# Kernel tuning notes

Measured on AMD Instinct MI355X. Metric: run time of the kernel, lower is better.

The kernel has to match this reference:

```python
import jax, jax.numpy as jnp
import numpy as np

B = 49152  # batch, divisible by 3 so each class has exactly B//3 samples
D = 512    # embedding dim
MARGIN1 = 0.5
MARGIN2 = 1.0


def setup_inputs() -> dict:
    key = jax.random.key(0)
    k1, k2 = jax.random.split(key)
    true_label = jnp.arange(B, dtype=jnp.int32) % 3  # equal class counts
    embedding = jax.random.normal(k1, (B, D), dtype=jnp.float32)
    proto = jax.random.normal(k2, (D,), dtype=jnp.float32)
    return {"true_label": true_label, "embedding": embedding, "proto": proto}


def reference(true_label, embedding, proto):
    count = true_label.shape[0] // 3  # static: labels are balanced by construction
    # per-sample squared distance to the prototype: d_i = ||proto - e_i||^2, shape [B]
    d = jnp.sum((proto[None, :] - embedding) ** 2, axis=-1)
    # fixed-size index gathers (jit-compatible since each class has exactly `count` members)
    i0 = jnp.nonzero(true_label == 0, size=count)[0]
    i1 = jnp.nonzero(true_label == 1, size=count)[0]
    i2 = jnp.nonzero(true_label == 2, size=count)[0]
    d1, d2, d3 = d[i0], d[i1], d[i2]  # each [count]
    loss = (jax.nn.relu(d1 - d2 + MARGIN1)
            + jax.nn.relu(d2 - d3 + MARGIN1)
            + jax.nn.relu(d1 - d3 + MARGIN2))
    # loop summed per-cc scalar losses then divided by count == mean
    return jnp.mean(loss)
```

## Files before the change

kernel.cpp:

```cpp
#include <hip/hip_runtime.h>

#define MARGIN1 0.5f
#define MARGIN2 1.0f

__global__ __launch_bounds__(256) void soso_main_kernel(
    const int* __restrict__ lab,
    const float* __restrict__ emb,
    const float* __restrict__ proto,
    float* __restrict__ partial,
    int ngroups)
{
    const int lane = threadIdx.x & 63;
    const int wid  = threadIdx.x >> 6;
    const int wavesPerGrid = gridDim.x * 4;
    const int gwave = blockIdx.x * 4 + wid;

    const float4 p0 = *reinterpret_cast<const float4*>(proto + 4 * lane);
    const float4 p1 = *reinterpret_cast<const float4*>(proto + 256 + 4 * lane);

    float acc = 0.0f;

    for (int g = gwave; g < ngroups; g += wavesPerGrid) {
        const float* base = emb + (size_t)g * 3u * 512u;
        float dsum[3];
#pragma unroll
        for (int r = 0; r < 3; ++r) {
            const float* row = base + r * 512;
            const float4 e0 = *reinterpret_cast<const float4*>(row + 4 * lane);
            const float4 e1 = *reinterpret_cast<const float4*>(row + 256 + 4 * lane);
            float s = 0.0f, t;
            t = p0.x - e0.x; s = fmaf(t, t, s);
            t = p0.y - e0.y; s = fmaf(t, t, s);
            t = p0.z - e0.z; s = fmaf(t, t, s);
            t = p0.w - e0.w; s = fmaf(t, t, s);
            t = p1.x - e1.x; s = fmaf(t, t, s);
            t = p1.y - e1.y; s = fmaf(t, t, s);
            t = p1.z - e1.z; s = fmaf(t, t, s);
            t = p1.w - e1.w; s = fmaf(t, t, s);
#pragma unroll
            for (int off = 32; off > 0; off >>= 1)
                s += __shfl_xor(s, off, 64);
            dsum[r] = s;
        }
        const int l0 = lab[3 * g + 0];
        const int l1 = lab[3 * g + 1];
        const int l2 = lab[3 * g + 2];
        const float d1 = (l0 == 0) ? dsum[0] : (l1 == 0) ? dsum[1] : dsum[2];
        const float d2 = (l0 == 1) ? dsum[0] : (l1 == 1) ? dsum[1] : dsum[2];
        const float d3 = (l0 == 2) ? dsum[0] : (l1 == 2) ? dsum[1] : dsum[2];

        acc += fmaxf(d1 - d2 + MARGIN1, 0.0f)
             + fmaxf(d2 - d3 + MARGIN1, 0.0f)
             + fmaxf(d1 - d3 + MARGIN2, 0.0f);
    }

    __shared__ float smem[4];
    if (lane == 0) smem[wid] = acc;
    __syncthreads();
    if (threadIdx.x == 0)
        partial[blockIdx.x] = smem[0] + smem[1] + smem[2] + smem[3];
}

__global__ __launch_bounds__(256) void soso_reduce_kernel(
    const float* __restrict__ partial,
    float* __restrict__ out,
    int n,
    float inv_count)
{
    float s = 0.0f;
    for (int i = threadIdx.x; i < n; i += 256)
        s += partial[i];
#pragma unroll
    for (int off = 32; off > 0; off >>= 1)
        s += __shfl_xor(s, off, 64);
    __shared__ float smem[4];
    if ((threadIdx.x & 63) == 0) smem[threadIdx.x >> 6] = s;
    __syncthreads();
    if (threadIdx.x == 0)
        out[0] = (smem[0] + smem[1] + smem[2] + smem[3]) * inv_count;
}

extern "C" void kernel_launch(void* const* d_in, const int* in_sizes, int n_in,
                              void* d_out, int out_size, void* d_ws, size_t ws_size,
                              hipStream_t stream)
{
    const int*   lab   = (const int*)d_in[0];
    const float* emb   = (const float*)d_in[1];
    const float* proto = (const float*)d_in[2];
    float* out = (float*)d_out;

    const int B = in_sizes[0];
    const int ngroups = B / 3;

    float* partial = (float*)d_ws;
    const int blocks = 2048;

    soso_main_kernel<<<blocks, 256, 0, stream>>>(lab, emb, proto, partial, ngroups);
    soso_reduce_kernel<<<1, 256, 0, stream>>>(partial, out, blocks,
                                              1.0f / (float)ngroups);
}
```

Before: 23.35 us.

## Replace two-kernel reduction with atomicAdd and launch one wave per two groups

Drops the second reduction kernel. Each block now atomically adds its scaled partial sum into the output, which is zeroed with a memset beforehand. The grid-stride loop becomes a fixed mapping of two groups per wave with a grid sized to the problem (2048 blocks), and launch bounds now request 8 blocks per CU. This removes a kernel launch and the serial tail reduction, in exchange for a memset node and 2048 atomics contending on a single address, plus a float summation order that is no longer deterministic.

```diff
diff --git a/kernel.cpp b/kernel.cpp
--- a/kernel.cpp
+++ b/kernel.cpp
@@ -3,81 +3,68 @@
 #define MARGIN1 0.5f
 #define MARGIN2 1.0f
 
-__global__ __launch_bounds__(256) void soso_main_kernel(
+__global__ __launch_bounds__(256, 8) void soso_main_kernel(
     const int* __restrict__ lab,
     const float* __restrict__ emb,
     const float* __restrict__ proto,
-    float* __restrict__ partial,
-    int ngroups)
+    float* __restrict__ out,
+    int ngroups,
+    float inv_count)
 {
-    const int lane = threadIdx.x & 63;
-    const int wid  = threadIdx.x >> 6;
-    const int wavesPerGrid = gridDim.x * 4;
+    const int lane  = threadIdx.x & 63;
+    const int wid   = threadIdx.x >> 6;
     const int gwave = blockIdx.x * 4 + wid;
+    const int g0    = gwave * 2;
 
     const float4 p0 = *reinterpret_cast<const float4*>(proto + 4 * lane);
     const float4 p1 = *reinterpret_cast<const float4*>(proto + 256 + 4 * lane);
 
     float acc = 0.0f;
 
-    for (int g = gwave; g < ngroups; g += wavesPerGrid) {
-        const float* base = emb + (size_t)g * 3u * 512u;
-        float dsum[3];
 #pragma unroll
-        for (int r = 0; r < 3; ++r) {
-            const float* row = base + r * 512;
-            const float4 e0 = *reinterpret_cast<const float4*>(row + 4 * lane);
-            const float4 e1 = *reinterpret_cast<const float4*>(row + 256 + 4 * lane);
-            float s = 0.0f, t;
-            t = p0.x - e0.x; s = fmaf(t, t, s);
-            t = p0.y - e0.y; s = fmaf(t, t, s);
-            t = p0.z - e0.z; s = fmaf(t, t, s);
-            t = p0.w - e0.w; s = fmaf(t, t, s);
-            t = p1.x - e1.x; s = fmaf(t, t, s);
-            t = p1.y - e1.y; s = fmaf(t, t, s);
-            t = p1.z - e1.z; s = fmaf(t, t, s);
-            t = p1.w - e1.w; s = fmaf(t, t, s);
+    for (int gg = 0; gg < 2; ++gg) {
+        const int g = g0 + gg;
+        if (g < ngroups) {
+            const float* base = emb + (size_t)g * 1536u;
+            float ds[3];
 #pragma unroll
-            for (int off = 32; off > 0; off >>= 1)
-                s += __shfl_xor(s, off, 64);
-            dsum[r] = s;
+            for (int r = 0; r < 3; ++r) {
+                const float* row = base + r * 512;
+                const float4 e0 = *reinterpret_cast<const float4*>(row + 4 * lane);
+                const float4 e1 = *reinterpret_cast<const float4*>(row + 256 + 4 * lane);
+                float s = 0.0f, t;
+                t = p0.x - e0.x; s = fmaf(t, t, s);
+                t = p0.y - e0.y; s = fmaf(t, t, s);
+                t = p0.z - e0.z; s = fmaf(t, t, s);
+                t = p0.w - e0.w; s = fmaf(t, t, s);
+                t = p1.x - e1.x; s = fmaf(t, t, s);
+                t = p1.y - e1.y; s = fmaf(t, t, s);
+                t = p1.z - e1.z; s = fmaf(t, t, s);
+                t = p1.w - e1.w; s = fmaf(t, t, s);
+#pragma unroll
+                for (int off = 32; off > 0; off >>= 1)
+                    s += __shfl_xor(s, off, 64);
+                ds[r] = s;
+            }
+            const int l0 = lab[3 * g + 0];
+            const int l1 = lab[3 * g + 1];
+            const float d1 = (l0 == 0) ? ds[0] : (l1 == 0) ? ds[1] : ds[2];
+            const float d2 = (l0 == 1) ? ds[0] : (l1 == 1) ? ds[1] : ds[2];
+            const float d3 = (l0 == 2) ? ds[0] : (l1 == 2) ? ds[1] : ds[2];
+
+            acc += fmaxf(d1 - d2 + MARGIN1, 0.0f)
+                 + fmaxf(d2 - d3 + MARGIN1, 0.0f)
+                 + fmaxf(d1 - d3 + MARGIN2, 0.0f);
         }
-        const int l0 = lab[3 * g + 0];
-        const int l1 = lab[3 * g + 1];
-        const int l2 = lab[3 * g + 2];
-        const float d1 = (l0 == 0) ? dsum[0] : (l1 == 0) ? dsum[1] : dsum[2];
-        const float d2 = (l0 == 1) ? dsum[0] : (l1 == 1) ? dsum[1] : dsum[2];
-        const float d3 = (l0 == 2) ? dsum[0] : (l1 == 2) ? dsum[1] : dsum[2];
-
-        acc += fmaxf(d1 - d2 + MARGIN1, 0.0f)
-             + fmaxf(d2 - d3 + MARGIN1, 0.0f)
-             + fmaxf(d1 - d3 + MARGIN2, 0.0f);
     }
 
     __shared__ float smem[4];
     if (lane == 0) smem[wid] = acc;
     __syncthreads();
-    if (threadIdx.x == 0)
-        partial[blockIdx.x] = smem[0] + smem[1] + smem[2] + smem[3];
-}
-
-__global__ __launch_bounds__(256) void soso_reduce_kernel(
-    const float* __restrict__ partial,
-    float* __restrict__ out,
-    int n,
-    float inv_count)
-{
-    float s = 0.0f;
-    for (int i = threadIdx.x; i < n; i += 256)
-        s += partial[i];
-#pragma unroll
-    for (int off = 32; off > 0; off >>= 1)
-        s += __shfl_xor(s, off, 64);
-    __shared__ float smem[4];
-    if ((threadIdx.x & 63) == 0) smem[threadIdx.x >> 6] = s;
-    __syncthreads();
-    if (threadIdx.x == 0)
-        out[0] = (smem[0] + smem[1] + smem[2] + smem[3]) * inv_count;
+    if (threadIdx.x == 0) {
+        const float blockSum = (smem[0] + smem[1] + smem[2] + smem[3]) * inv_count;
+        atomicAdd(out, blockSum);
+    }
 }
 
 extern "C" void kernel_launch(void* const* d_in, const int* in_sizes, int n_in,
@@ -91,11 +78,11 @@
 
     const int B = in_sizes[0];
     const int ngroups = B / 3;
+    const int waves   = (ngroups + 1) / 2;
+    const int blocks  = (waves + 3) / 4;
 
-    float* partial = (float*)d_ws;
-    const int blocks = 2048;
+    hipMemsetAsync(out, 0, sizeof(float), stream);
 
-    soso_main_kernel<<<blocks, 256, 0, stream>>>(lab, emb, proto, partial, ngroups);
-    soso_reduce_kernel<<<1, 256, 0, stream>>>(partial, out, blocks,
-                                              1.0f / (float)ngroups);
+    soso_main_kernel<<<blocks, 256, 0, stream>>>(lab, emb, proto, out,
+                                                 ngroups, 1.0f / (float)ngroups);
 }
```

Result: slower. 42.28 us (+81.1%).

## Assign two groups per wave, batch loads, and interleave the three row reductions

Applied to the files above, without the earlier changes.

Replaces the grid-stride loop with a fixed two-groups-per-wave mapping. The grid is now sized from the problem (about 2048 blocks for this batch) instead of a fixed 2048. Each group issues all six row loads up front and runs the three butterfly reductions interleaved, which gives more memory-level parallelism and shortens shuffle dependency chains. Adds a launch_bounds occupancy hint of 8 blocks per SM. The reduce kernel now handles a problem-dependent partial count, which could grow large for bigger inputs.

```diff
diff --git a/kernel.cpp b/kernel.cpp
--- a/kernel.cpp
+++ b/kernel.cpp
@@ -3,55 +3,70 @@
 #define MARGIN1 0.5f
 #define MARGIN2 1.0f
 
-__global__ __launch_bounds__(256) void soso_main_kernel(
+__global__ __launch_bounds__(256, 8) void soso_main_kernel(
     const int* __restrict__ lab,
     const float* __restrict__ emb,
     const float* __restrict__ proto,
     float* __restrict__ partial,
     int ngroups)
 {
-    const int lane = threadIdx.x & 63;
-    const int wid  = threadIdx.x >> 6;
-    const int wavesPerGrid = gridDim.x * 4;
+    const int lane  = threadIdx.x & 63;
+    const int wid   = threadIdx.x >> 6;
     const int gwave = blockIdx.x * 4 + wid;
+    const int g0    = gwave * 2;
 
     const float4 p0 = *reinterpret_cast<const float4*>(proto + 4 * lane);
     const float4 p1 = *reinterpret_cast<const float4*>(proto + 256 + 4 * lane);
 
     float acc = 0.0f;
 
-    for (int g = gwave; g < ngroups; g += wavesPerGrid) {
-        const float* base = emb + (size_t)g * 3u * 512u;
-        float dsum[3];
 #pragma unroll
-        for (int r = 0; r < 3; ++r) {
-            const float* row = base + r * 512;
-            const float4 e0 = *reinterpret_cast<const float4*>(row + 4 * lane);
-            const float4 e1 = *reinterpret_cast<const float4*>(row + 256 + 4 * lane);
-            float s = 0.0f, t;
-            t = p0.x - e0.x; s = fmaf(t, t, s);
-            t = p0.y - e0.y; s = fmaf(t, t, s);
-            t = p0.z - e0.z; s = fmaf(t, t, s);
-            t = p0.w - e0.w; s = fmaf(t, t, s);
-            t = p1.x - e1.x; s = fmaf(t, t, s);
-            t = p1.y - e1.y; s = fmaf(t, t, s);
-            t = p1.z - e1.z; s = fmaf(t, t, s);
-            t = p1.w - e1.w; s = fmaf(t, t, s);
+    for (int gg = 0; gg < 2; ++gg) {
+        const int g = g0 + gg;
+        if (g < ngroups) {
+            const float* base = emb + (size_t)g * 1536u;
+
+            float4 e0[3], e1[3];
 #pragma unroll
-            for (int off = 32; off > 0; off >>= 1)
-                s += __shfl_xor(s, off, 64);
-            dsum[r] = s;
+            for (int r = 0; r < 3; ++r) {
+                const float* row = base + r * 512;
+                e0[r] = *reinterpret_cast<const float4*>(row + 4 * lane);
+                e1[r] = *reinterpret_cast<const float4*>(row + 256 + 4 * lane);
+            }
+
+            float s[3];
+#pragma unroll
+            for (int r = 0; r < 3; ++r) {
+                float v = 0.0f, t;
+                t = p0.x - e0[r].x; v = fmaf(t, t, v);
+                t = p0.y - e0[r].y; v = fmaf(t, t, v);
+                t = p0.z - e0[r].z; v = fmaf(t, t, v);
+                t = p0.w - e0[r].w; v = fmaf(t, t, v);
+                t = p1.x - e1[r].x; v = fmaf(t, t, v);
+                t = p1.y - e1[r].y; v = fmaf(t, t, v);
+                t = p1.z - e1[r].z; v = fmaf(t, t, v);
+                t = p1.w - e1[r].w; v = fmaf(t, t, v);
+                s[r] = v;
+            }
+
+#pragma unroll
+            for (int off = 32; off > 0; off >>= 1) {
+                const float t0 = __shfl_xor(s[0], off, 64);
+                const float t1 = __shfl_xor(s[1], off, 64);
+                const float t2 = __shfl_xor(s[2], off, 64);
+                s[0] += t0; s[1] += t1; s[2] += t2;
+            }
+
+            const int l0 = lab[3 * g + 0];
+            const int l1 = lab[3 * g + 1];
+            const float d1 = (l0 == 0) ? s[0] : (l1 == 0) ? s[1] : s[2];
+            const float d2 = (l0 == 1) ? s[0] : (l1 == 1) ? s[1] : s[2];
+            const float d3 = (l0 == 2) ? s[0] : (l1 == 2) ? s[1] : s[2];
+
+            acc += fmaxf(d1 - d2 + MARGIN1, 0.0f)
+                 + fmaxf(d2 - d3 + MARGIN1, 0.0f)
+                 + fmaxf(d1 - d3 + MARGIN2, 0.0f);
         }
-        const int l0 = lab[3 * g + 0];
-        const int l1 = lab[3 * g + 1];
-        const int l2 = lab[3 * g + 2];
-        const float d1 = (l0 == 0) ? dsum[0] : (l1 == 0) ? dsum[1] : dsum[2];
-        const float d2 = (l0 == 1) ? dsum[0] : (l1 == 1) ? dsum[1] : dsum[2];
-        const float d3 = (l0 == 2) ? dsum[0] : (l1 == 2) ? dsum[1] : dsum[2];
-
-        acc += fmaxf(d1 - d2 + MARGIN1, 0.0f)
-             + fmaxf(d2 - d3 + MARGIN1, 0.0f)
-             + fmaxf(d1 - d3 + MARGIN2, 0.0f);
     }
 
     __shared__ float smem[4];
@@ -91,9 +106,10 @@
 
     const int B = in_sizes[0];
     const int ngroups = B / 3;
+    const int waves   = (ngroups + 1) / 2;
+    const int blocks  = (waves + 3) / 4;
 
     float* partial = (float*)d_ws;
-    const int blocks = 2048;
 
     soso_main_kernel<<<blocks, 256, 0, stream>>>(lab, emb, proto, partial, ngroups);
     soso_reduce_kernel<<<1, 256, 0, stream>>>(partial, out, blocks,
```

New measurement: 23.14 us. No clear change (-0.9%).
